# Kernel optimization log

Hardware: AMD Instinct MI355X
Metric: run time of the kernel (lower is better)

Reference implementation:

```python
import jax, jax.numpy as jnp
import numpy as np

B, D, E, H, A = 4096, 1024, 8, 1024, 512  # batch, state_dim, num_options, num_neurons, num_actions


def setup_inputs() -> dict:
    key = jax.random.key(0)
    ks = jax.random.split(key, 16)
    s = 0.02
    return {
        "state": jax.random.normal(ks[0], (B, D), jnp.float32),
        "selected_options": jax.random.randint(ks[1], (B,), 0, E, jnp.int32),
        # option network: Linear(D,H) -> ReLU -> Linear(H,E)
        "Wo1": jax.random.normal(ks[2], (D, H), jnp.float32) * s,
        "bo1": jnp.zeros((H,), jnp.float32),
        "Wo2": jax.random.normal(ks[3], (H, E), jnp.float32) * s,
        "bo2": jnp.zeros((E,), jnp.float32),
        # E expert nets, each: Linear(D,H)+ReLU -> Linear(H,H)+ReLU -> Linear(H,A)
        "We1": jax.random.normal(ks[4], (E, D, H), jnp.float32) * s,
        "be1": jnp.zeros((E, H), jnp.float32),
        "We2": jax.random.normal(ks[5], (E, H, H), jnp.float32) * s,
        "be2": jnp.zeros((E, H), jnp.float32),
        "We3": jax.random.normal(ks[6], (E, H, A), jnp.float32) * s,
        "be3": jnp.zeros((E, A), jnp.float32),
        # termination network: Linear(D,H) -> ReLU -> Linear(H,1) -> Sigmoid
        "Wt1": jax.random.normal(ks[7], (D, H), jnp.float32) * s,
        "bt1": jnp.zeros((H,), jnp.float32),
        "Wt2": jax.random.normal(ks[8], (H, 1), jnp.float32) * s,
        "bt2": jnp.zeros((1,), jnp.float32),
    }


def reference(state, selected_options, Wo1, bo1, Wo2, bo2,
              We1, be1, We2, be2, We3, be3, Wt1, bt1, Wt2, bt2):
    # option head
    option_probs = jax.nn.softmax(jnp.maximum(state @ Wo1 + bo1, 0.0) @ Wo2 + bo2, axis=-1)

    # expert MLPs: compute all experts vectorized, then gather per-sample selected expert.
    # (the torch code loops per sample; equal action sizes so no padding is needed)
    h = jnp.maximum(jnp.einsum("bd,edh->beh", state, We1) + be1, 0.0)   # [B,E,H]
    h = jnp.maximum(jnp.einsum("beh,ehk->bek", h, We2) + be2, 0.0)      # [B,E,H]
    logits = jnp.einsum("beh,eha->bea", h, We3) + be3                   # [B,E,A]
    probs_all = jax.nn.softmax(logits, axis=-1)
    sel = selected_options[:, None, None]
    action_probs = jnp.take_along_axis(probs_all, sel, axis=1)[:, 0, :]  # [B,A]
    selected_actions = jnp.argmax(action_probs, axis=-1)

    # termination head
    termination_prob = jax.nn.sigmoid(jnp.maximum(state @ Wt1 + bt1, 0.0) @ Wt2 + bt2)

    return option_probs, action_probs, termination_prob, selected_options, selected_actions
```

## Files before the change

### kernel.cpp

```cpp
#include <hip/hip_runtime.h>
#include <hip/hip_bf16.h>

#define B_ 4096
#define D_ 1024
#define E_ 8
#define H_ 1024
#define A_ 512
#define PB 6144
#define NTT 24
#define FB_CAP 128
#define FROWS (E_ * FB_CAP)
#define KSPLIT 4
#define MARGIN 3.0e-3f

typedef __attribute__((ext_vector_type(8))) short s16x8;
typedef __attribute__((ext_vector_type(4))) float f32x4;

__device__ __forceinline__ unsigned short f2bf(float f) {
    __hip_bfloat16 h = __float2bfloat16(f);
    return *reinterpret_cast<unsigned short*>(&h);
}
__device__ __forceinline__ float bf2f(unsigned short u) {
    return __uint_as_float(((unsigned int)u) << 16);
}
__device__ __forceinline__ void gload16(const void* g, void* l) {
    __builtin_amdgcn_global_load_lds(
        (const __attribute__((address_space(1))) unsigned int*)g,
        (__attribute__((address_space(3))) unsigned int*)l, 16, 0, 0);
}

__device__ __forceinline__ int a_src_chunk(int lane) { return (((lane & 7) ^ (lane >> 3)) * 8); }

__device__ __forceinline__ int trc(int r, int c) { return (c + r + (r >> 2)) & 63; }

__device__ __forceinline__ void tr_tile_256(const float* __restrict__ src, int Nsrc,
                                            unsigned short* __restrict__ dst, float* T) {
    const int t = threadIdx.x;
    const int c4 = (t & 15) * 4, r0 = t >> 4;
#pragma unroll
    for (int i = 0; i < 8; ++i) {
        const int r = r0 + i * 16;
        const float4 v = *(const float4*)&src[(size_t)r * Nsrc + c4];
        float* Tr = T + r * 64;
        Tr[trc(r, c4 + 0)] = v.x; Tr[trc(r, c4 + 1)] = v.y;
        Tr[trc(r, c4 + 2)] = v.z; Tr[trc(r, c4 + 3)] = v.w;
    }
    __syncthreads();
    const int k4 = (t & 31) * 4, n0 = t >> 5;
#pragma unroll
    for (int i = 0; i < 8; ++i) {
        const int n = n0 + i * 8;
        ushort4 o;
        o.x = f2bf(T[(k4 + 0) * 64 + trc(k4 + 0, n)]);
        o.y = f2bf(T[(k4 + 1) * 64 + trc(k4 + 1, n)]);
        o.z = f2bf(T[(k4 + 2) * 64 + trc(k4 + 2, n)]);
        o.w = f2bf(T[(k4 + 3) * 64 + trc(k4 + 3, n)]);
        *(ushort4*)&dst[(size_t)n * 1024 + k4] = o;
    }
}

__device__ __forceinline__ int t32idx(int k, int c2) {
    return k * 64 + ((c2 + 5 * (k >> 3) + k) & 63);
}
__device__ __forceinline__ void tr_tile_128x128_w512(const float* __restrict__ src, int Nsrc,
                                                     unsigned short* __restrict__ dst,
                                                     unsigned int* T32) {
    const int t = threadIdx.x;
#pragma unroll
    for (int i = 0; i < 8; ++i) {
        const int id = t + i * 512;
        const int r  = id >> 5;
        const int c4 = (id & 31) * 4;
        const float4 v = *(const float4*)&src[(size_t)r * Nsrc + c4];
        const unsigned int u0 = (unsigned)f2bf(v.x) | ((unsigned)f2bf(v.y) << 16);
        const unsigned int u1 = (unsigned)f2bf(v.z) | ((unsigned)f2bf(v.w) << 16);
        T32[t32idx(r, (c4 >> 1) + 0)] = u0;
        T32[t32idx(r, (c4 >> 1) + 1)] = u1;
    }
    __syncthreads();
#pragma unroll
    for (int q = 0; q < 4; ++q) {
        const int id = t + q * 512;
        const int n = id >> 4;
        const int L = id & 15;
        const int hi = n & 1;
        unsigned int w[4];
#pragma unroll
        for (int jj = 0; jj < 4; ++jj) {
            const int k0 = L * 8 + 2 * jj;
            const unsigned int a = T32[t32idx(k0,     n >> 1)];
            const unsigned int b = T32[t32idx(k0 + 1, n >> 1)];
            const unsigned int ha = hi ? (a >> 16) : (a & 0xffffu);
            const unsigned int hb = hi ? (b >> 16) : (b & 0xffffu);
            w[jj] = ha | (hb << 16);
        }
        *(uint4*)&dst[(size_t)n * 1024 + L * 8] = make_uint4(w[0], w[1], w[2], w[3]);
    }
}

__global__ void k_prep(const float* __restrict__ x, unsigned short* __restrict__ y,
                       const float* __restrict__ Wo1, const float* __restrict__ Wt1,
                       unsigned short* __restrict__ Wbf,
                       const float* __restrict__ We1, unsigned short* __restrict__ We1t,
                       const int* __restrict__ sel, int* __restrict__ tile_expert,
                       int* __restrict__ rowlist, int* __restrict__ pos_of_row,
                       int* __restrict__ rowlist2, int* __restrict__ cur2) {
    __shared__ float T[128 * 64];
    const int t = threadIdx.x;
    const int bid = blockIdx.x;
    if (bid >= 4353) {
        const int q = bid - 4353;
        const int e = q >> 7, r = q & 127, kt = r >> 4, ntb = r & 15;
        tr_tile_256(We1 + (size_t)e * 1048576 + (size_t)(kt * 128) * 1024 + ntb * 64, 1024,
                    We1t + (size_t)e * 1048576 + (size_t)(ntb * 64) * 1024 + kt * 128, T);
        return;
    }
    if (bid >= 4097) {
        const int q = bid - 4097;
        const int m = q >> 7, r = q & 127, kt = r >> 4, ntb = r & 15;
        const float* src = (m ? Wt1 : Wo1) + (size_t)(kt * 128) * 1024 + ntb * 64;
        tr_tile_256(src, 1024, Wbf + (size_t)(m * 1024 + ntb * 64) * 1024 + kt * 128, T);
        return;
    }
    if (bid > 0) {
        int i = (bid - 1) * 256 + t;
        float4 v = ((const float4*)x)[i];
        ushort4 o;
        o.x = f2bf(v.x); o.y = f2bf(v.y); o.z = f2bf(v.z); o.w = f2bf(v.w);
        ((ushort4*)y)[i] = o;
        return;
    }
    __shared__ int scnt[E_], soff[E_], scur[E_];
    if (t < E_) { scnt[t] = 0; scur[t] = 0; cur2[t] = 0; }
    for (int i = t; i < PB; i += 256) rowlist[i] = -1;
    for (int i = t; i < FROWS; i += 256) rowlist2[i] = -1;
    __syncthreads();
    for (int b = t; b < B_; b += 256) {
        int e = sel[b]; e = e < 0 ? 0 : (e >= E_ ? E_ - 1 : e);
        atomicAdd(&scnt[e], 1);
    }
    __syncthreads();
    if (t == 0) {
        int off = 0;
        for (int e = 0; e < E_; ++e) {
            soff[e] = off;
            int tiles = (scnt[e] + 255) >> 8;
            for (int k = 0; k < tiles; ++k) tile_expert[(off >> 8) + k] = e;
            off += tiles << 8;
        }
        for (int k = off >> 8; k < NTT; ++k) tile_expert[k] = -1;
    }
    __syncthreads();
    for (int b = t; b < B_; b += 256) {
        int e = sel[b]; e = e < 0 ? 0 : (e >= E_ ? E_ - 1 : e);
        int pos = atomicAdd(&scur[e], 1);
        int p = soff[e] + pos; if (p >= PB) p = PB - 1;
        rowlist[p] = b;
        pos_of_row[b] = p;
    }
}

template<int TN>
__device__ __forceinline__ void gemm3(
    const unsigned short* __restrict__ g0, const unsigned short* __restrict__ g1,
    const unsigned short* __restrict__ g2, const unsigned short* __restrict__ g3,
    const unsigned short* __restrict__ Bt, int Kg, const float* __restrict__ bp,
    unsigned short* __restrict__ Cbf, float* __restrict__ Cf, int Ncols, int relu,
    unsigned short* As, unsigned short* Bs)
{
    constexpr int NI = TN / 32;
    constexpr int BTH = TN * 64;
    constexpr int BR = TN / 64;
    const int t = threadIdx.x, lane = t & 63, w = t >> 6;
    const int wr = w >> 1, wc = w & 1;
    const int aseg = w * 2048 + lane * 8;
    const int bseg = w * (BR * 512) + lane * 8;
    const int coffb = a_src_chunk(lane);
    const unsigned short* bsrc = Bt + (size_t)(w * BR * 8 + (lane >> 3)) * Kg + coffb;

    f32x4 acc[4][NI];
#pragma unroll
    for (int i = 0; i < 4; ++i)
#pragma unroll
        for (int j = 0; j < NI; ++j)
#pragma unroll
            for (int r = 0; r < 4; ++r) acc[i][j][r] = 0.f;

#define G_STAGE(IT, BUF) {                                                   \
        const int ko_ = (IT) * 64;                                           \
        const int oa_ = (BUF) * 16384 + aseg;                                \
        gload16(g0 + ko_, As + oa_);                                         \
        gload16(g1 + ko_, As + oa_ + 512);                                   \
        gload16(g2 + ko_, As + oa_ + 1024);                                  \
        gload16(g3 + ko_, As + oa_ + 1536);                                  \
        const int ob_ = (BUF) * BTH + bseg;                                  \
        _Pragma("unroll")                                                    \
        for (int j_ = 0; j_ < BR; ++j_)                                      \
            gload16(bsrc + ko_ + (size_t)(j_ * 8) * Kg, Bs + ob_ + j_ * 512); \
    }

    G_STAGE(0, 0);
    __syncthreads();

    for (int it = 0; it < 16; ++it) {
        const int cb = it & 1;
        if (it + 1 < 16) G_STAGE(it + 1, cb ^ 1);
        __builtin_amdgcn_s_setprio(1);
#pragma unroll
        for (int kq = 0; kq < 2; ++kq) {
            const int sc = kq * 4 + (lane >> 4);
            s16x8 af[4], bfr[NI];
#pragma unroll
            for (int mi = 0; mi < 4; ++mi) {
                const int ar = wr * 64 + mi * 16 + (lane & 15);
                af[mi] = *reinterpret_cast<const s16x8*>(
                    &As[cb * 16384 + ar * 64 + ((sc ^ (ar & 7)) << 3)]);
            }
#pragma unroll
            for (int ni = 0; ni < NI; ++ni) {
                const int br = wc * (TN / 2) + ni * 16 + (lane & 15);
                bfr[ni] = *reinterpret_cast<const s16x8*>(
                    &Bs[cb * BTH + br * 64 + ((sc ^ (br & 7)) << 3)]);
            }
#pragma unroll
            for (int mi = 0; mi < 4; ++mi)
#pragma unroll
                for (int ni = 0; ni < NI; ++ni)
                    acc[mi][ni] = __builtin_amdgcn_mfma_f32_16x16x32_bf16(
                        af[mi], bfr[ni], acc[mi][ni], 0, 0, 0);
        }
        __builtin_amdgcn_s_setprio(0);
        if (it + 1 < 16) __syncthreads();
    }
#undef G_STAGE

    const int cq = lane >> 4, cr = lane & 15;
#pragma unroll
    for (int ni = 0; ni < NI; ++ni) {
        const int col_l = wc * (TN / 2) + ni * 16 + cr;
        const float bv = bp[col_l];
#pragma unroll
        for (int mi = 0; mi < 4; ++mi) {
#pragma unroll
            for (int r = 0; r < 4; ++r) {
                const int row_l = wr * 64 + mi * 16 + cq * 4 + r;
                float v = acc[mi][ni][r] + bv;
                if (relu) v = fmaxf(v, 0.f);
                const size_t idx = (size_t)row_l * Ncols + col_l;
                if (Cbf) Cbf[idx] = f2bf(v);
                if (Cf)  Cf[idx] = v;
            }
        }
    }
}

__global__ __launch_bounds__(512, 2)
void k_d2(const unsigned short* __restrict__ Sbf,
          const int* __restrict__ rowlist, const int* __restrict__ tile_expert,
          const unsigned short* __restrict__ Wbf,
          const float* __restrict__ bo1, const float* __restrict__ bt1,
          const unsigned short* __restrict__ We1t, const float* __restrict__ be1,
          const float* __restrict__ We2, unsigned short* __restrict__ We2t,
          unsigned short* __restrict__ hopt, unsigned short* __restrict__ hterm,
          unsigned short* __restrict__ h1) {
    __shared__ __align__(16) unsigned short SMEM[4 * 16384];
    unsigned short* As = SMEM;
    unsigned short* Bs = SMEM + 2 * 16384;
    const int bid = blockIdx.x;
    const int t = threadIdx.x, lane = t & 63, w = t >> 6;
    const int coff = a_src_chunk(lane);
    const int r0l = w * 32 + (lane >> 3);

    if (bid < 128) {
        const int nt = bid & 7, mt = bid >> 3;
        const unsigned short* g0 = Sbf + (size_t)(mt * 256 + r0l) * D_ + coff;
        const unsigned short* g1 = g0 + (size_t)8 * D_;
        const unsigned short* g2 = g0 + (size_t)16 * D_;
        const unsigned short* g3 = g0 + (size_t)24 * D_;
        int ntRow; const float* bp; unsigned short* C;
        if (nt < 4) { ntRow = nt * 256; bp = bo1 + nt * 256;
                      C = hopt + (size_t)(mt * 256) * H_ + nt * 256; }
        else { ntRow = 1024 + (nt - 4) * 256; bp = bt1 + (nt - 4) * 256;
               C = hterm + (size_t)(mt * 256) * H_ + (nt - 4) * 256; }
        gemm3<256>(g0, g1, g2, g3, Wbf + (size_t)ntRow * 1024, 1024, bp,
                   C, nullptr, H_, 1, As, Bs);
    } else {
        const int q = bid - 128, nt = q & 3, mt = q >> 2;
        const int e = tile_expert[mt];
        if (e >= 0) {
            const int base = mt * 256;
            const int sub = rowlist[base];
            if (sub >= 0) {
                int r0 = rowlist[base + r0l];      if (r0 < 0) r0 = sub;
                int r1 = rowlist[base + r0l + 8];  if (r1 < 0) r1 = sub;
                int r2 = rowlist[base + r0l + 16]; if (r2 < 0) r2 = sub;
                int r3 = rowlist[base + r0l + 24]; if (r3 < 0) r3 = sub;
                const unsigned short* g0 = Sbf + (size_t)r0 * D_ + coff;
                const unsigned short* g1 = Sbf + (size_t)r1 * D_ + coff;
                const unsigned short* g2 = Sbf + (size_t)r2 * D_ + coff;
                const unsigned short* g3 = Sbf + (size_t)r3 * D_ + coff;
                gemm3<256>(g0, g1, g2, g3,
                           We1t + (size_t)e * 1048576 + (size_t)(nt * 256) * 1024, 1024,
                           be1 + (size_t)e * H_ + nt * 256,
                           h1 + (size_t)(mt * 256) * H_ + nt * 256, nullptr, H_, 1, As, Bs);
            }
        }
    }

    for (int q = bid; q < 512; q += 224) {
        __syncthreads();
        const int e = q >> 6, r = q & 63, kt = r >> 3, ntb = r & 7;
        tr_tile_128x128_w512(We2 + (size_t)e * 1048576 + (size_t)(kt * 128) * 1024 + ntb * 128, 1024,
                             We2t + (size_t)e * 1048576 + (size_t)(ntb * 128) * 1024 + kt * 128,
                             (unsigned int*)SMEM);
    }
}

__global__ __launch_bounds__(512, 2)
void k_d3(const unsigned short* __restrict__ h1, const int* __restrict__ tile_expert,
          const unsigned short* __restrict__ We2t, const float* __restrict__ be2,
          const float* __restrict__ We3, unsigned short* __restrict__ We3t,
          unsigned short* __restrict__ h2) {
    __shared__ __align__(16) unsigned short SMEM[2 * 16384 + 2 * 8192];
    unsigned short* As = SMEM;
    unsigned short* Bs = SMEM + 2 * 16384;
    const int bid = blockIdx.x;
    const int t = threadIdx.x, lane = t & 63, w = t >> 6;
    const int coff = a_src_chunk(lane);
    const int r0l = w * 32 + (lane >> 3);

    {
        const int nt = bid & 7, mt = bid >> 3;
        const int e = tile_expert[mt];
        if (e >= 0) {
            const unsigned short* g0 = h1 + (size_t)(mt * 256 + r0l) * H_ + coff;
            gemm3<128>(g0, g0 + (size_t)8 * H_, g0 + (size_t)16 * H_, g0 + (size_t)24 * H_,
                       We2t + (size_t)e * 1048576 + (size_t)(nt * 128) * 1024, 1024,
                       be2 + (size_t)e * H_ + nt * 128,
                       h2 + (size_t)(mt * 256) * H_ + nt * 128, nullptr, H_, 1, As, Bs);
        }
    }

    for (int q = bid; q < 256; q += 192) {
        __syncthreads();
        const int e = q >> 5, r = q & 31, kt = r >> 2, ntb = r & 3;
        tr_tile_128x128_w512(We3 + (size_t)e * 524288 + (size_t)(kt * 128) * 512 + ntb * 128, 512,
                             We3t + (size_t)e * 524288 + (size_t)(ntb * 128) * 1024 + kt * 128,
                             (unsigned int*)SMEM);
    }
}

__global__ __launch_bounds__(512, 2)
void k_d5(const unsigned short* __restrict__ h2, const int* __restrict__ tile_expert,
          const unsigned short* __restrict__ We3t, const float* __restrict__ be3,
          float* __restrict__ lgt) {
    __shared__ __align__(16) unsigned short SMEM[2 * 16384 + 2 * 4096];
    unsigned short* As = SMEM;
    unsigned short* Bs = SMEM + 2 * 16384;
    const int t = threadIdx.x, lane = t & 63, w = t >> 6;
    const int coff = a_src_chunk(lane);
    const int r0l = w * 32 + (lane >> 3);
    const int nt = blockIdx.x & 7, mt = blockIdx.x >> 3;
    const int e = tile_expert[mt]; if (e < 0) return;
    const unsigned short* g0 = h2 + (size_t)(mt * 256 + r0l) * H_ + coff;
    gemm3<64>(g0, g0 + (size_t)8 * H_, g0 + (size_t)16 * H_, g0 + (size_t)24 * H_,
              We3t + (size_t)e * 524288 + (size_t)(nt * 64) * 1024, 1024,
              be3 + (size_t)e * A_ + nt * 64,
              nullptr, lgt + (size_t)(mt * 256) * A_ + nt * 64, A_, 0, As, Bs);
}

__device__ __forceinline__ void opt_body(int b, const unsigned short* __restrict__ h,
                                         const float* __restrict__ Wo2, const float* __restrict__ bo2,
                                         float* __restrict__ out, float* sm) {
    const int t = threadIdx.x;
    float acc[E_];
#pragma unroll
    for (int j = 0; j < E_; ++j) acc[j] = 0.f;
    for (int k = t; k < H_; k += 256) {
        float hv = bf2f(h[(size_t)b * H_ + k]);
#pragma unroll
        for (int j = 0; j < E_; ++j) acc[j] = fmaf(hv, Wo2[k * E_ + j], acc[j]);
    }
#pragma unroll
    for (int j = 0; j < E_; ++j)
        for (int off = 32; off; off >>= 1) acc[j] += __shfl_down(acc[j], off, 64);
    float* red = sm;
    float* probs = sm + 4 * E_;
    int wave = t >> 6, lane = t & 63;
    if (lane == 0)
        for (int j = 0; j < E_; ++j) red[wave * E_ + j] = acc[j];
    __syncthreads();
    if (t == 0) {
        float z[E_]; float m = -1e30f;
        for (int j = 0; j < E_; ++j) {
            z[j] = red[j] + red[E_ + j] + red[2 * E_ + j] + red[3 * E_ + j] + bo2[j];
            m = fmaxf(m, z[j]);
        }
        float s = 0.f;
        for (int j = 0; j < E_; ++j) { z[j] = expf(z[j] - m); s += z[j]; }
        float inv = 1.f / s;
        for (int j = 0; j < E_; ++j) probs[j] = z[j] * inv;
    }
    __syncthreads();
    if (t < E_) out[(size_t)b * E_ + t] = probs[t];
}

__device__ __forceinline__ void term_body(int b, const unsigned short* __restrict__ h,
                                          const float* __restrict__ Wt2, const float* __restrict__ bt2,
                                          float* __restrict__ out, float* sm) {
    const int t = threadIdx.x;
    float acc = 0.f;
    for (int k = t; k < H_; k += 256) acc = fmaf(bf2f(h[(size_t)b * H_ + k]), Wt2[k], acc);
    for (int off = 32; off; off >>= 1) acc += __shfl_down(acc, off, 64);
    if ((t & 63) == 0) sm[t >> 6] = acc;
    __syncthreads();
    if (t == 0) {
        float z = sm[0] + sm[1] + sm[2] + sm[3] + bt2[0];
        out[b] = 1.f / (1.f + expf(-z));
    }
}

__global__ __launch_bounds__(256)
void k_gather(const float* __restrict__ logits, const int* __restrict__ pos_of_row,
              const int* __restrict__ sel,
              float* __restrict__ out_probs, float* __restrict__ out_selopt,
              float* __restrict__ out_selact,
              int* __restrict__ rowlist2, int* __restrict__ cur2,
              const unsigned short* __restrict__ hopt, const float* __restrict__ Wo2,
              const float* __restrict__ bo2, float* __restrict__ out_opt,
              const unsigned short* __restrict__ hterm, const float* __restrict__ Wt2,
              const float* __restrict__ bt2, float* __restrict__ out_term) {
    __shared__ float smbuf[5 * E_ + 8];
    const int bid = blockIdx.x;
    if (bid >= 2 * B_) { term_body(bid - 2 * B_, hterm, Wt2, bt2, out_term, smbuf); return; }
    if (bid >= B_)     { opt_body(bid - B_, hopt, Wo2, bo2, out_opt, smbuf); return; }

    const int b = bid;
    int p = pos_of_row[b];
    if (p < 0) p = 0; if (p >= PB) p = PB - 1;
    const int t = threadIdx.x;
    const float* L = logits + (size_t)p * A_;
    float v0 = L[t], v1 = L[t + 256];

    float bv; int bi;
    if (v0 >= v1) { bv = v0; bi = t; } else { bv = v1; bi = t + 256; }
    for (int off = 32; off; off >>= 1) {
        float ov = __shfl_down(bv, off, 64);
        int   oi = __shfl_down(bi, off, 64);
        if (ov > bv || (ov == bv && oi < bi)) { bv = ov; bi = oi; }
    }
    __shared__ float rv[4]; __shared__ int ri[4];
    int wave = t >> 6, lane = t & 63;
    if (lane == 0) { rv[wave] = bv; ri[wave] = bi; }
    __syncthreads();
    __shared__ float sM; __shared__ int sBi;
    if (t == 0) {
        float mv = rv[0]; int mi = ri[0];
        for (int w = 1; w < 4; ++w)
            if (rv[w] > mv || (rv[w] == mv && ri[w] < mi)) { mv = rv[w]; mi = ri[w]; }
        sM = mv; sBi = mi;
    }
    __syncthreads();
    const float M = sM; const int BI = sBi;

    float e0 = expf(v0 - M), e1 = expf(v1 - M);
    float s = e0 + e1;
    for (int off = 32; off; off >>= 1) s += __shfl_down(s, off, 64);
    __shared__ float reds[4];
    if (lane == 0) reds[wave] = s;
    __syncthreads();
    float inv = 1.f / (reds[0] + reds[1] + reds[2] + reds[3]);

    out_probs[(size_t)b * A_ + t]       = e0 * inv;
    out_probs[(size_t)b * A_ + t + 256] = e1 * inv;

    float s0 = (t == BI) ? -1e30f : v0;
    float s1 = (t + 256 == BI) ? -1e30f : v1;
    float sm = fmaxf(s0, s1);
    for (int off = 32; off; off >>= 1) sm = fmaxf(sm, __shfl_down(sm, off, 64));
    __shared__ float red2[4];
    if (lane == 0) red2[wave] = sm;
    __syncthreads();

    if (t == 0) {
        float second = fmaxf(fmaxf(red2[0], red2[1]), fmaxf(red2[2], red2[3]));
        out_selact[b] = (float)BI;
        int e = sel[b]; e = e < 0 ? 0 : (e >= E_ ? E_ - 1 : e);
        out_selopt[b] = (float)sel[b];
        if (M - second < MARGIN) {
            int pos = atomicAdd(&cur2[e], 1);
            if (pos < FB_CAP) rowlist2[e * FB_CAP + pos] = b;
        }
    }
}

#define BM 64
#define BN 64
#define BK 32

__global__ __launch_bounds__(256)
void k_pgemm(const float* __restrict__ A, int lda, const int* __restrict__ flags,
             int gather, const float* __restrict__ W,
             float* __restrict__ P, int K, int N) {
    __shared__ float As_[BK][BM + 4];
    __shared__ float Bs_[BK][BN];

    const int mt = blockIdx.y, nt = blockIdx.x, kz = blockIdx.z;
    if (flags[mt * BM] < 0) return;
    const int e = mt >> 1;
    const float* Wb = W + (size_t)e * K * N + (size_t)nt * BN;

    const int t  = threadIdx.x;
    const int tx = t & 15;
    const int ty = t >> 4;

    const int arow = t >> 3;
    const int ak   = (t & 7) * 4;
    int r0 = mt * BM + arow, r1 = r0 + 32;
    if (gather) { r0 = flags[r0]; r1 = flags[r1]; }
    const int bkr = t >> 4;
    const int bn  = (t & 15) * 4;

    float acc[4][4];
#pragma unroll
    for (int i = 0; i < 4; ++i)
#pragma unroll
        for (int j = 0; j < 4; ++j) acc[i][j] = 0.0f;

    const int kbeg = kz * (K / KSPLIT);
    const int kend = kbeg + (K / KSPLIT);
    for (int k0 = kbeg; k0 < kend; k0 += BK) {
        float4 a0 = make_float4(0.f, 0.f, 0.f, 0.f), a1 = a0;
        if (r0 >= 0) a0 = *(const float4*)&A[(size_t)r0 * lda + k0 + ak];
        if (r1 >= 0) a1 = *(const float4*)&A[(size_t)r1 * lda + k0 + ak];
        float4 b0 = *(const float4*)&Wb[(size_t)(k0 + bkr) * N + bn];
        float4 b1 = *(const float4*)&Wb[(size_t)(k0 + bkr + 16) * N + bn];

        __syncthreads();
        As_[ak + 0][arow] = a0.x; As_[ak + 1][arow] = a0.y;
        As_[ak + 2][arow] = a0.z; As_[ak + 3][arow] = a0.w;
        As_[ak + 0][arow + 32] = a1.x; As_[ak + 1][arow + 32] = a1.y;
        As_[ak + 2][arow + 32] = a1.z; As_[ak + 3][arow + 32] = a1.w;
        *(float4*)&Bs_[bkr][bn]      = b0;
        *(float4*)&Bs_[bkr + 16][bn] = b1;
        __syncthreads();

#pragma unroll
        for (int kk = 0; kk < BK; ++kk) {
            const float4 av = *(const float4*)&As_[kk][ty * 4];
            const float4 bv = *(const float4*)&Bs_[kk][tx * 4];
            const float a_[4] = {av.x, av.y, av.z, av.w};
            const float b_[4] = {bv.x, bv.y, bv.z, bv.w};
#pragma unroll
            for (int i = 0; i < 4; ++i)
#pragma unroll
                for (int j = 0; j < 4; ++j)
                    acc[i][j] = fmaf(a_[i], b_[j], acc[i][j]);
        }
    }

    float* Pz = P + (size_t)kz * FROWS * N;
    const int n0 = nt * BN + tx * 4;
#pragma unroll
    for (int i = 0; i < 4; ++i) {
        int m = mt * BM + ty * 4 + i;
        *(float4*)&Pz[(size_t)m * N + n0] = make_float4(acc[i][0], acc[i][1], acc[i][2], acc[i][3]);
    }
}

__global__ __launch_bounds__(256)
void k_fred(const float* __restrict__ P, const int* __restrict__ flags,
            const float* __restrict__ bias, float* __restrict__ C, int N, int relu) {
    const int m = blockIdx.x;
    if (flags[m] < 0) return;
    const int e = m >> 7;
    const int t = threadIdx.x;
    if (t * 4 >= N) return;
    const size_t MN = (size_t)FROWS * N;
    const size_t base = (size_t)m * N + t * 4;
    float4 s = *(const float4*)&P[base];
#pragma unroll
    for (int z = 1; z < KSPLIT; ++z) {
        float4 p = *(const float4*)&P[(size_t)z * MN + base];
        s.x += p.x; s.y += p.y; s.z += p.z; s.w += p.w;
    }
    const float* bp = bias + (size_t)e * N + t * 4;
    s.x += bp[0]; s.y += bp[1]; s.z += bp[2]; s.w += bp[3];
    if (relu) {
        s.x = fmaxf(s.x, 0.f); s.y = fmaxf(s.y, 0.f);
        s.z = fmaxf(s.z, 0.f); s.w = fmaxf(s.w, 0.f);
    }
    *(float4*)&C[base] = s;
}

__global__ __launch_bounds__(256)
void k_fixup(const float* __restrict__ logitsf, const int* __restrict__ rowlist2,
             float* __restrict__ out_probs, float* __restrict__ out_selact) {
    const int i = blockIdx.x;
    const int row = rowlist2[i];
    if (row < 0) return;
    const int t = threadIdx.x;
    const float* L = logitsf + (size_t)i * A_;
    float v0 = L[t], v1 = L[t + 256];

    float bv; int bi;
    if (v0 >= v1) { bv = v0; bi = t; } else { bv = v1; bi = t + 256; }
    for (int off = 32; off; off >>= 1) {
        float ov = __shfl_down(bv, off, 64);
        int   oi = __shfl_down(bi, off, 64);
        if (ov > bv || (ov == bv && oi < bi)) { bv = ov; bi = oi; }
    }
    __shared__ float rv[4]; __shared__ int ri[4];
    int wave = t >> 6, lane = t & 63;
    if (lane == 0) { rv[wave] = bv; ri[wave] = bi; }
    __syncthreads();
    __shared__ float sM; __shared__ int sBi;
    if (t == 0) {
        float mv = rv[0]; int mi = ri[0];
        for (int w = 1; w < 4; ++w)
            if (rv[w] > mv || (rv[w] == mv && ri[w] < mi)) { mv = rv[w]; mi = ri[w]; }
        sM = mv; sBi = mi;
    }
    __syncthreads();

    float e0 = expf(v0 - sM), e1 = expf(v1 - sM);
    float s = e0 + e1;
    for (int off = 32; off; off >>= 1) s += __shfl_down(s, off, 64);
    __shared__ float reds[4];
    if (lane == 0) reds[wave] = s;
    __syncthreads();
    float inv = 1.f / (reds[0] + reds[1] + reds[2] + reds[3]);

    out_probs[(size_t)row * A_ + t]       = e0 * inv;
    out_probs[(size_t)row * A_ + t + 256] = e1 * inv;
    if (t == 0) out_selact[row] = (float)sBi;
}

extern "C" void kernel_launch(void* const* d_in, const int* in_sizes, int n_in,
                              void* d_out, int out_size, void* d_ws, size_t ws_size,
                              hipStream_t stream) {
    const float* state = (const float*)d_in[0];
    const int*   sel   = (const int*)d_in[1];
    const float* Wo1 = (const float*)d_in[2];
    const float* bo1 = (const float*)d_in[3];
    const float* Wo2 = (const float*)d_in[4];
    const float* bo2 = (const float*)d_in[5];
    const float* We1 = (const float*)d_in[6];
    const float* be1 = (const float*)d_in[7];
    const float* We2 = (const float*)d_in[8];
    const float* be2 = (const float*)d_in[9];
    const float* We3 = (const float*)d_in[10];
    const float* be3 = (const float*)d_in[11];
    const float* Wt1 = (const float*)d_in[12];
    const float* bt1 = (const float*)d_in[13];
    const float* Wt2 = (const float*)d_in[14];
    const float* bt2 = (const float*)d_in[15];
    float* out = (float*)d_out;

    char* w = (char*)d_ws;
    int* meta        = (int*)w;
    int* rowlist     = meta;
    int* pos_of_row  = meta + 6144;
    int* rowlist2    = meta + 10240;
    int* tile_expert = meta + 11264;
    int* cur2        = meta + 11296;
    char* P0 = w + 65536;
    char* P1 = P0 + 12582912;
    char* P2 = P1 + 16777216;
    char* W1 = P2 + 12582912;
    char* W2 = W1 + 16777216;
    unsigned short* Sbf   = (unsigned short*)P0;
    unsigned short* Wbf   = (unsigned short*)(P0 + (8u << 20));
    unsigned short* h2b   = (unsigned short*)P0;
    unsigned short* hopt  = (unsigned short*)P1;
    unsigned short* hterm = hopt + (size_t)B_ * H_;
    unsigned short* h1b   = (unsigned short*)P2;
    unsigned short* We1t  = (unsigned short*)W1;
    unsigned short* We3t  = (unsigned short*)W1;
    unsigned short* We2t  = (unsigned short*)W2;
    float* lgt  = (float*)P2;
    float* Pbuf = (float*)P1;
    float* h1f  = (float*)P0;
    float* h2f  = h1f + (size_t)FROWS * H_;
    float* lgf  = h2f + (size_t)FROWS * H_;

    size_t act_off    = (size_t)B_ * E_;
    size_t term_off   = act_off + (size_t)B_ * A_;
    size_t selopt_off = term_off + B_;
    size_t selact_off = selopt_off + B_;

    k_prep<<<5377, 256, 0, stream>>>(state, Sbf, Wo1, Wt1, Wbf, We1, We1t,
                                     sel, tile_expert, rowlist, pos_of_row, rowlist2, cur2);

    k_d2<<<224, 512, 0, stream>>>(Sbf, rowlist, tile_expert, Wbf,
                                  bo1, bt1, We1t, be1, We2, We2t, hopt, hterm, h1b);
    k_d3<<<192, 512, 0, stream>>>(h1b, tile_expert, We2t, be2, We3, We3t, h2b);
    k_d5<<<192, 512, 0, stream>>>(h2b, tile_expert, We3t, be3, lgt);

    k_gather<<<3 * B_, 256, 0, stream>>>(lgt, pos_of_row, sel,
                                         out + act_off, out + selopt_off, out + selact_off,
                                         rowlist2, cur2,
                                         hopt, Wo2, bo2, out,
                                         hterm, Wt2, bt2, out + term_off);

    k_pgemm<<<dim3(H_ / BN, FROWS / BM, KSPLIT), 256, 0, stream>>>(state, D_, rowlist2, 1, We1, Pbuf, D_, H_);
    k_fred<<<FROWS, 256, 0, stream>>>(Pbuf, rowlist2, be1, h1f, H_, 1);
    k_pgemm<<<dim3(H_ / BN, FROWS / BM, KSPLIT), 256, 0, stream>>>(h1f, H_, rowlist2, 0, We2, Pbuf, H_, H_);
    k_fred<<<FROWS, 256, 0, stream>>>(Pbuf, rowlist2, be2, h2f, H_, 1);
    k_pgemm<<<dim3(A_ / BN, FROWS / BM, KSPLIT), 256, 0, stream>>>(h2f, H_, rowlist2, 0, We3, Pbuf, H_, A_);
    k_fred<<<FROWS, 256, 0, stream>>>(Pbuf, rowlist2, be3, lgf, A_, 0);
    k_fixup<<<FROWS, 256, 0, stream>>>(lgf, rowlist2, out + act_off, out + selact_off);
}
```

Measured before the change: 217.9 us.

## Split weight transposes into separate blocks and use fine-grained vmcnt waits in GEMM

The weight-transpose work for We2 and We3, previously done in a loop after each block's GEMM, now runs in dedicated extra blocks of k_d2 and k_d3. These blocks can overlap with the GEMM blocks instead of extending their tail. The GEMM main loop replaces __syncthreads with explicit s_waitcnt vmcnt counts and raw s_barrier, so the next stage's global loads can stay in flight while the current tile is computed. The explicit waitcnt values depend on the exact number of loads per thread, which is fragile if the load count or compiler scheduling changes.

```diff
diff --git a/kernel.cpp b/kernel.cpp
--- a/kernel.cpp
+++ b/kernel.cpp
@@ -171,6 +171,7 @@
     constexpr int NI = TN / 32;
     constexpr int BTH = TN * 64;
     constexpr int BR = TN / 64;
+    constexpr int LPT = 4 + BR;
     const int t = threadIdx.x, lane = t & 63, w = t >> 6;
     const int wr = w >> 1, wc = w & 1;
     const int aseg = w * 2048 + lane * 8;
@@ -200,11 +201,19 @@
     }
 
     G_STAGE(0, 0);
-    __syncthreads();
 
     for (int it = 0; it < 16; ++it) {
         const int cb = it & 1;
-        if (it + 1 < 16) G_STAGE(it + 1, cb ^ 1);
+        if (it + 1 < 16) {
+            G_STAGE(it + 1, cb ^ 1);
+            if constexpr (LPT == 8)      asm volatile("s_waitcnt vmcnt(8)" ::: "memory");
+            else if constexpr (LPT == 6) asm volatile("s_waitcnt vmcnt(6)" ::: "memory");
+            else                         asm volatile("s_waitcnt vmcnt(5)" ::: "memory");
+        } else {
+            asm volatile("s_waitcnt vmcnt(0)" ::: "memory");
+        }
+        __builtin_amdgcn_s_barrier();
+        __builtin_amdgcn_sched_barrier(0);
         __builtin_amdgcn_s_setprio(1);
 #pragma unroll
         for (int kq = 0; kq < 2; ++kq) {
@@ -230,7 +239,11 @@
                         af[mi], bfr[ni], acc[mi][ni], 0, 0, 0);
         }
         __builtin_amdgcn_s_setprio(0);
-        if (it + 1 < 16) __syncthreads();
+        if (it + 1 < 16) {
+            asm volatile("s_waitcnt lgkmcnt(0)" ::: "memory");
+            __builtin_amdgcn_sched_barrier(0);
+            __builtin_amdgcn_s_barrier();
+        }
     }
 #undef G_STAGE
 
@@ -267,10 +280,17 @@
     unsigned short* As = SMEM;
     unsigned short* Bs = SMEM + 2 * 16384;
     const int bid = blockIdx.x;
+    if (bid >= 224) {
+        const int q = bid - 224;
+        const int e = q >> 6, r = q & 63, kt = r >> 3, ntb = r & 7;
+        tr_tile_128x128_w512(We2 + (size_t)e * 1048576 + (size_t)(kt * 128) * 1024 + ntb * 128, 1024,
+                             We2t + (size_t)e * 1048576 + (size_t)(ntb * 128) * 1024 + kt * 128,
+                             (unsigned int*)SMEM);
+        return;
+    }
     const int t = threadIdx.x, lane = t & 63, w = t >> 6;
     const int coff = a_src_chunk(lane);
     const int r0l = w * 32 + (lane >> 3);
-
     if (bid < 128) {
         const int nt = bid & 7, mt = bid >> 3;
         const unsigned short* g0 = Sbf + (size_t)(mt * 256 + r0l) * D_ + coff;
@@ -286,33 +306,21 @@
                    C, nullptr, H_, 1, As, Bs);
     } else {
         const int q = bid - 128, nt = q & 3, mt = q >> 2;
-        const int e = tile_expert[mt];
-        if (e >= 0) {
-            const int base = mt * 256;
-            const int sub = rowlist[base];
-            if (sub >= 0) {
-                int r0 = rowlist[base + r0l];      if (r0 < 0) r0 = sub;
-                int r1 = rowlist[base + r0l + 8];  if (r1 < 0) r1 = sub;
-                int r2 = rowlist[base + r0l + 16]; if (r2 < 0) r2 = sub;
-                int r3 = rowlist[base + r0l + 24]; if (r3 < 0) r3 = sub;
-                const unsigned short* g0 = Sbf + (size_t)r0 * D_ + coff;
-                const unsigned short* g1 = Sbf + (size_t)r1 * D_ + coff;
-                const unsigned short* g2 = Sbf + (size_t)r2 * D_ + coff;
-                const unsigned short* g3 = Sbf + (size_t)r3 * D_ + coff;
-                gemm3<256>(g0, g1, g2, g3,
-                           We1t + (size_t)e * 1048576 + (size_t)(nt * 256) * 1024, 1024,
-                           be1 + (size_t)e * H_ + nt * 256,
-                           h1 + (size_t)(mt * 256) * H_ + nt * 256, nullptr, H_, 1, As, Bs);
-            }
-        }
-    }
-
-    for (int q = bid; q < 512; q += 224) {
-        __syncthreads();
-        const int e = q >> 6, r = q & 63, kt = r >> 3, ntb = r & 7;
-        tr_tile_128x128_w512(We2 + (size_t)e * 1048576 + (size_t)(kt * 128) * 1024 + ntb * 128, 1024,
-                             We2t + (size_t)e * 1048576 + (size_t)(ntb * 128) * 1024 + kt * 128,
-                             (unsigned int*)SMEM);
+        const int e = tile_expert[mt]; if (e < 0) return;
+        const int base = mt * 256;
+        const int sub = rowlist[base]; if (sub < 0) return;
+        int r0 = rowlist[base + r0l];      if (r0 < 0) r0 = sub;
+        int r1 = rowlist[base + r0l + 8];  if (r1 < 0) r1 = sub;
+        int r2 = rowlist[base + r0l + 16]; if (r2 < 0) r2 = sub;
+        int r3 = rowlist[base + r0l + 24]; if (r3 < 0) r3 = sub;
+        const unsigned short* g0 = Sbf + (size_t)r0 * D_ + coff;
+        const unsigned short* g1 = Sbf + (size_t)r1 * D_ + coff;
+        const unsigned short* g2 = Sbf + (size_t)r2 * D_ + coff;
+        const unsigned short* g3 = Sbf + (size_t)r3 * D_ + coff;
+        gemm3<256>(g0, g1, g2, g3,
+                   We1t + (size_t)e * 1048576 + (size_t)(nt * 256) * 1024, 1024,
+                   be1 + (size_t)e * H_ + nt * 256,
+                   h1 + (size_t)(mt * 256) * H_ + nt * 256, nullptr, H_, 1, As, Bs);
     }
 }
 
@@ -325,29 +333,24 @@
     unsigned short* As = SMEM;
     unsigned short* Bs = SMEM + 2 * 16384;
     const int bid = blockIdx.x;
-    const int t = threadIdx.x, lane = t & 63, w = t >> 6;
-    const int coff = a_src_chunk(lane);
-    const int r0l = w * 32 + (lane >> 3);
-
-    {
-        const int nt = bid & 7, mt = bid >> 3;
-        const int e = tile_expert[mt];
-        if (e >= 0) {
-            const unsigned short* g0 = h1 + (size_t)(mt * 256 + r0l) * H_ + coff;
-            gemm3<128>(g0, g0 + (size_t)8 * H_, g0 + (size_t)16 * H_, g0 + (size_t)24 * H_,
-                       We2t + (size_t)e * 1048576 + (size_t)(nt * 128) * 1024, 1024,
-                       be2 + (size_t)e * H_ + nt * 128,
-                       h2 + (size_t)(mt * 256) * H_ + nt * 128, nullptr, H_, 1, As, Bs);
-        }
-    }
-
-    for (int q = bid; q < 256; q += 192) {
-        __syncthreads();
+    if (bid >= 192) {
+        const int q = bid - 192;
         const int e = q >> 5, r = q & 31, kt = r >> 2, ntb = r & 3;
         tr_tile_128x128_w512(We3 + (size_t)e * 524288 + (size_t)(kt * 128) * 512 + ntb * 128, 512,
                              We3t + (size_t)e * 524288 + (size_t)(ntb * 128) * 1024 + kt * 128,
                              (unsigned int*)SMEM);
-    }
+        return;
+    }
+    const int t = threadIdx.x, lane = t & 63, w = t >> 6;
+    const int coff = a_src_chunk(lane);
+    const int r0l = w * 32 + (lane >> 3);
+    const int nt = bid & 7, mt = bid >> 3;
+    const int e = tile_expert[mt]; if (e < 0) return;
+    const unsigned short* g0 = h1 + (size_t)(mt * 256 + r0l) * H_ + coff;
+    gemm3<128>(g0, g0 + (size_t)8 * H_, g0 + (size_t)16 * H_, g0 + (size_t)24 * H_,
+               We2t + (size_t)e * 1048576 + (size_t)(nt * 128) * 1024, 1024,
+               be2 + (size_t)e * H_ + nt * 128,
+               h2 + (size_t)(mt * 256) * H_ + nt * 128, nullptr, H_, 1, As, Bs);
 }
 
 __global__ __launch_bounds__(512, 2)
@@ -692,9 +695,9 @@
     k_prep<<<5377, 256, 0, stream>>>(state, Sbf, Wo1, Wt1, Wbf, We1, We1t,
                                      sel, tile_expert, rowlist, pos_of_row, rowlist2, cur2);
 
-    k_d2<<<224, 512, 0, stream>>>(Sbf, rowlist, tile_expert, Wbf,
+    k_d2<<<736, 512, 0, stream>>>(Sbf, rowlist, tile_expert, Wbf,
                                   bo1, bt1, We1t, be1, We2, We2t, hopt, hterm, h1b);
-    k_d3<<<192, 512, 0, stream>>>(h1b, tile_expert, We2t, be2, We3, We3t, h2b);
+    k_d3<<<448, 512, 0, stream>>>(h1b, tile_expert, We2t, be2, We3, We3t, h2b);
     k_d5<<<192, 512, 0, stream>>>(h2b, tile_expert, We3t, be3, lgt);
 
     k_gather<<<3 * B_, 256, 0, stream>>>(lgt, pos_of_row, sel,
```

Result: faster. 210.3 us (-3.5%).
